# Kernel optimization log

Measured on AMD Instinct MI355X. Metric: run time of the kernel, lower is better.

## Reference

```python
import jax, jax.numpy as jnp
import numpy as np

N, C, L = 1024, 3, 6000
CONV_CH = [20, 32, 64, 20]
K = 3            # conv kernel size, padding (K-1)//2 = 1 -> SAME
POOL = 2
HID = 100
FLAT_DIM = (L // POOL**4 + 2 * C + 1) * CONV_CH[-1]  # (375 + 7) * 20 = 7640


def setup_inputs() -> dict:
    key = jax.random.key(0)
    ks = jax.random.split(key, 10)
    d = {"x": jax.random.normal(ks[0], (N, C, L), jnp.float32)}
    ins = [C] + CONV_CH[:-1]
    for i, (ic, oc) in enumerate(zip(ins, CONV_CH)):
        d[f"w{i}"] = jax.random.normal(ks[1 + i], (oc, ic, K), jnp.float32) * (1.0 / np.sqrt(ic * K))
        d[f"b{i}"] = jnp.zeros((oc,), jnp.float32)
    d["wc"] = jax.random.normal(ks[6], (CONV_CH[-1], C, 1), jnp.float32) * (1.0 / np.sqrt(C))
    d["bc"] = jnp.zeros((CONV_CH[-1],), jnp.float32)
    d["wl0"] = jax.random.normal(ks[7], (HID, FLAT_DIM), jnp.float32) * (1.0 / np.sqrt(FLAT_DIM))
    d["bl0"] = jnp.zeros((HID,), jnp.float32)
    d["wl1"] = jax.random.normal(ks[8], (2, HID), jnp.float32) * (1.0 / np.sqrt(HID))
    d["bl1"] = jnp.zeros((2,), jnp.float32)
    return d


def conv1d(x, w, b, pad):
    # x: (N, C_in, L), w: (C_out, C_in, K)
    out = jax.lax.conv_general_dilated(x, w, (1,), [(pad, pad)],
                                       dimension_numbers=('NCH', 'OIH', 'NCH'))
    return out + b[None, :, None]


def maxpool2(x):
    n, c, l = x.shape  # l always even here (6000 / 2^k)
    return x.reshape(n, c, l // 2, 2).max(-1)


def cov_eig_feats(x):
    # batched covariance as a single contraction (avoids the O(N*L*C*C) bmm intermediate)
    n, c, l = x.shape
    diff = x - x.mean(-1, keepdims=True)
    cov = jnp.einsum('ncl,ndl->ncd', diff, diff) / (l - 1)  # (N, C, C)
    # cov is symmetric PSD -> eigh (real); torch uses generic eig and keeps real parts
    vals, vecs = jnp.linalg.eigh(cov)
    vals = vals[..., None] / vals.max()          # global max over batch, like torch
    cov = cov / jnp.abs(cov).max()
    return jnp.concatenate([cov, vals, vecs], axis=-1)  # (N, C, 2C+1)


def reference(x, w0, b0, w1, b1, w2, b2, w3, b3, wc, bc, wl0, bl0, wl1, bl1):
    feats = jax.lax.stop_gradient(cov_eig_feats(x))  # torch branch is @no_grad
    h = x
    for w, b in ((w0, b0), (w1, b1), (w2, b2), (w3, b3)):
        h = maxpool2(jax.nn.relu(conv1d(h, w, b, (K - 1) // 2)))
    h = h.reshape(h.shape[0], -1)                    # (N, 20*375)
    h1 = jax.nn.relu(conv1d(feats, wc, bc, 0))       # (N, 20, 7)
    h1 = h1.reshape(h1.shape[0], -1)
    h = jnp.concatenate([h, h1], axis=1)             # (N, 7640)
    h = jax.nn.relu(h @ wl0.T + bl0)
    out = h @ wl1.T + bl1                            # (N, 2)
    return (out[:, :1], out[:, 1:])
```

## Files before the change

### kernel.cpp

```cpp
#include <hip/hip_runtime.h>
#include <hip/hip_bf16.h>
#include <hip/hip_fp16.h>
#include <math.h>

#define NBATCH 1024
#define LIN    6000
#define HCATW  7640
#define HID    100

#define TCH   54
#define NCHK  7

#define ASZ 3552
#define BSZ 8920

#define W0OFF 0
#define W1OFF 192
#define W2OFF 2112
#define W3OFF 8256
#define B0OFF 12352
#define B1OFF 12372
#define B2OFF 12404
#define B3OFF 12468
#define WREPSZ 12496

#define FCNS 4

__device__ __forceinline__ void pack_one(int idx, int OC, int IC, int OCG,
                                         int OPG, int WSTR,
                                         const float* __restrict__ w,
                                         float* __restrict__ dst)
{
    if (idx >= OCG * IC * WSTR) return;
    int ocg = idx / (IC * WSTR);
    int r   = idx - ocg * (IC * WSTR);
    int ic  = r / WSTR;
    int q   = r - ic * WSTR;
    int o   = q / 3, k = q - o * 3;
    int oc  = ocg * OPG + o;
    dst[idx] = (o < OPG && oc < OC) ? w[(oc * IC + ic) * 3 + k] : 0.f;
}

__global__ __launch_bounds__(256) void repack_kernel(
    const float* __restrict__ w0, const float* __restrict__ b0,
    const float* __restrict__ w1, const float* __restrict__ b1,
    const float* __restrict__ w2, const float* __restrict__ b2,
    const float* __restrict__ w3, const float* __restrict__ b3,
    float* __restrict__ wrep)
{
    int idx = blockIdx.x * 256 + threadIdx.x;
    pack_one(idx, 20,  3, 4, 5, 16, w0, wrep + W0OFF);
    pack_one(idx, 32, 20, 4, 8, 24, w1, wrep + W1OFF);
    pack_one(idx, 64, 32, 8, 8, 24, w2, wrep + W2OFF);
    pack_one(idx, 20, 64, 4, 5, 16, w3, wrep + W3OFF);
    if (idx < 20)            wrep[B0OFF + idx] = b0[idx];
    else if (idx < 52)  { int i = idx - 20;  wrep[B1OFF + i] = b1[i]; }
    else if (idx < 116) { int i = idx - 52;  wrep[B2OFF + i] = b2[i]; }
    else if (idx < 136) { int i = idx - 116; wrep[B3OFF + i] = b3[i]; }
}

template<int IC, int OC, int OCG, int OPG, int WSTR, int JOUT, int LG, int JBLK,
         bool IN16, bool OUT16, bool FINAL>
__device__ __forceinline__ void stage_eo(const float* __restrict__ in,
                                         float* __restrict__ out,
                                         float* __restrict__ outg,
                                         const float* __restrict__ wrep,
                                         const float* __restrict__ brep,
                                         int pbase, int o3, int wv, int lane,
                                         int zero)
{
    constexpr int PIN  = JOUT + 1;
    constexpr int POUT = JOUT / 2;
    constexpr int NJT  = (JOUT + 64 * JBLK - 1) / (64 * JBLK);
    for (int task = wv; task < OCG * NJT; task += 8) {
        const int ocg = task / NJT;
        const int jt  = task - ocg * NJT;
        const int j0  = jt * (64 * JBLK) + lane;
        const float* bp = brep + ocg * OPG;
        float ae[JBLK][OPG], ao[JBLK][OPG];
#pragma unroll
        for (int t = 0; t < JBLK; ++t)
#pragma unroll
            for (int o = 0; o < OPG; ++o) { ae[t][o] = bp[o]; ao[t][o] = ae[t][o]; }
        const float* wbase = wrep + ocg * (IC * WSTR) + zero;
#pragma unroll 2
        for (int ic = 0; ic < IC; ++ic) {
            const float* wp = wbase + ic * WSTR;
            float wr[WSTR];
#pragma unroll
            for (int q = 0; q < WSTR / 4; ++q)
                *(float4*)&wr[q * 4] = *(const float4*)(wp + q * 4);
#pragma unroll
            for (int t = 0; t < JBLK; ++t) {
                const int jj = j0 + t * 64;
                const int jc = (jj < JOUT) ? jj : (JOUT - 1);
                float e0, e1, o0, o1;
                if constexpr (IN16) {
                    const float* ipw = in + ic * PIN;
                    uint2 pw;
                    __builtin_memcpy(&pw, ipw + jc, 8);
                    __half2 h0 = *reinterpret_cast<const __half2*>(&pw.x);
                    __half2 h1 = *reinterpret_cast<const __half2*>(&pw.y);
                    e0 = __low2float(h0); o0 = __high2float(h0);
                    e1 = __low2float(h1); o1 = __high2float(h1);
                } else {
                    const float* ip = in + ic * (2 * PIN);
                    float2 ev, ov;
                    __builtin_memcpy(&ev, ip + jc, 8);
                    __builtin_memcpy(&ov, ip + PIN + jc, 8);
                    e0 = ev.x; e1 = ev.y;
                    o0 = ov.x; o1 = ov.y;
                }
#pragma unroll
                for (int o = 0; o < OPG; ++o) {
                    const float w0 = wr[o*3+0], w1 = wr[o*3+1], w2 = wr[o*3+2];
                    ae[t][o] = fmaf(e0, w0, fmaf(o0, w1, fmaf(e1, w2, ae[t][o])));
                    ao[t][o] = fmaf(o0, w0, fmaf(e1, w1, fmaf(o1, w2, ao[t][o])));
                }
            }
        }
#pragma unroll
        for (int t = 0; t < JBLK; ++t) {
            const int jj = j0 + t * 64;
            if constexpr (FINAL) {
                const int gj = o3 + jj;
                if (gj < 375 && jj < JOUT) {
#pragma unroll
                    for (int o = 0; o < OPG; ++o)
                        outg[(ocg*OPG+o) * 375 + gj] =
                            fmaxf(fmaxf(ae[t][o], ao[t][o]), 0.f);
                }
            } else {
                const int g = pbase + jj;
                const bool val = (jj < JOUT) && (g >= 0) && (g < LG);
                if (jj < JOUT) {
                    if constexpr (OUT16) {
                        __half* dh = (__half*)out;
#pragma unroll
                        for (int o = 0; o < OPG; ++o) {
                            float v = val ? fmaxf(fmaxf(ae[t][o], ao[t][o]), 0.f)
                                          : 0.f;
                            dh[(ocg*OPG+o) * JOUT + jj] = __float2half(v);
                        }
                    } else {
                        float* dst = out + ((jj & 1) ? POUT : 0) + (jj >> 1);
#pragma unroll
                        for (int o = 0; o < OPG; ++o)
                            dst[(ocg*OPG+o) * JOUT] =
                                val ? fmaxf(fmaxf(ae[t][o], ao[t][o]), 0.f) : 0.f;
                    }
                }
            }
        }
    }
}

__global__ __launch_bounds__(512, 6) void conv_chain_eo(
    const float* __restrict__ x,
    const float* __restrict__ wrep,
    float* __restrict__ hcat)
{
    __shared__ float A[ASZ];
    __shared__ float B[BSZ];

    const int tid  = threadIdx.x;
    const int wv   = __builtin_amdgcn_readfirstlane(tid >> 6);
    const int lane = tid & 63;
    const int zero = __builtin_amdgcn_ds_bpermute(0, 0);
    const int n     = blockIdx.x / NCHK;
    const int chunk = blockIdx.x % NCHK;
    const int o3 = chunk * TCH;
    const int p2 = 2*o3 - 1, p1 = 4*o3 - 3, p0 = 8*o3 - 7, xs = 16*o3 - 15;

    const float* xn = x + (size_t)n * 3 * LIN;
    for (int idx = tid; idx < 3 * 894; idx += 512) {
        int c = idx / 894, i = idx - c * 894;
        int g = xs + i;
        float v = (g >= 0 && g < LIN) ? xn[c * LIN + g] : 0.f;
        A[c * 894 + ((i & 1) ? 447 : 0) + (i >> 1)] = v;
    }
    __syncthreads();
    stage_eo< 3, 20, 4, 5, 16, 446, 3000, 2, false, false, false>(
        A, B, nullptr, wrep + W0OFF, wrep + B0OFF, p0, o3, wv, lane, zero);
    __syncthreads();
    stage_eo<20, 32, 4, 8, 24, 222, 1500, 2, false, true,  false>(
        B, A, nullptr, wrep + W1OFF, wrep + B1OFF, p1, o3, wv, lane, zero);
    __syncthreads();
    stage_eo<32, 64, 8, 8, 24, 110,  750, 2, true,  false, false>(
        A, B, nullptr, wrep + W2OFF, wrep + B2OFF, p2, o3, wv, lane, zero);
    __syncthreads();
    stage_eo<64, 20, 4, 5, 16,  54,  375, 1, false, false, true >(
        B, nullptr, hcat + (size_t)n * HCATW,
        wrep + W3OFF, wrep + B3OFF, o3, o3, wv, lane, zero);
}

__device__ __forceinline__ float fsign(float a, float b) {
    return (b >= 0.0f) ? fabsf(a) : -fabsf(a);
}
__device__ __forceinline__ float slapy2(float xx, float yy) {
    float xa = fabsf(xx), ya = fabsf(yy);
    float w = fmaxf(xa, ya), z = fminf(xa, ya);
    if (z == 0.f) return w;
    float t = z / w;
    return w * sqrtf(1.f + t*t);
}
__device__ __forceinline__ void slartg(float f, float g, float& c, float& s, float& r) {
    if (g == 0.f)      { c = 1.f; s = 0.f; r = f; }
    else if (f == 0.f) { c = 0.f; s = (g >= 0.f ? 1.f : -1.f); r = fabsf(g); }
    else {
        float d = sqrtf(f*f + g*g);
        c = fabsf(f) / d;
        r = fsign(d, f);
        s = g / r;
    }
}
__device__ void slaev2(float a, float b, float cc,
                       float& rt1, float& rt2, float& cs1, float& sn1) {
    float sm = a + cc, df = a - cc;
    float adf = fabsf(df);
    float tb = b + b, ab = fabsf(tb);
    float acmx, acmn;
    if (fabsf(a) > fabsf(cc)) { acmx = a; acmn = cc; } else { acmx = cc; acmn = a; }
    float rt;
    if (adf > ab)      { float t = ab/adf; rt = adf*sqrtf(1.f + t*t); }
    else if (adf < ab) { float t = adf/ab; rt = ab*sqrtf(1.f + t*t); }
    else rt = ab * sqrtf(2.f);
    int sgn1;
    if (sm < 0.f)      { rt1 = 0.5f*(sm - rt); sgn1 = -1; rt2 = (acmx/rt1)*acmn - (b/rt1)*b; }
    else if (sm > 0.f) { rt1 = 0.5f*(sm + rt); sgn1 =  1; rt2 = (acmx/rt1)*acmn - (b/rt1)*b; }
    else               { rt1 = 0.5f*rt; rt2 = -0.5f*rt; sgn1 = 1; }
    float cs; int sgn2;
    if (df >= 0.f) { cs = df + rt; sgn2 = 1; } else { cs = df - rt; sgn2 = -1; }
    float acs = fabsf(cs);
    if (acs > ab) {
        float ct = -tb / cs;
        sn1 = 1.f / sqrtf(1.f + ct*ct);
        cs1 = ct * sn1;
    } else {
        if (ab == 0.f) { cs1 = 1.f; sn1 = 0.f; }
        else {
            float tn = -cs / tb;
            cs1 = 1.f / sqrtf(1.f + tn*tn);
            sn1 = tn * cs1;
        }
    }
    if (sgn1 == sgn2) { float tn = cs1; cs1 = -sn1; sn1 = tn; }
}
__device__ __forceinline__ void rot_cols(float z[3][3], int jc, float c, float s) {
    for (int i = 0; i < 3; ++i) {
        float t = z[i][jc+1];
        z[i][jc+1] = c*t - s*z[i][jc];
        z[i][jc]   = s*t + c*z[i][jc];
    }
}

__device__ void ssteqr3(float d[3], float e[2], float z[3][3]) {
    const float eps    = 5.9604645e-8f;
    const float eps2   = eps * eps;
    const float safmin = 1.17549435e-38f;
    const int n = 3;
    for (int i = 0; i < 3; ++i)
        for (int j = 0; j < 3; ++j) z[i][j] = (i == j) ? 1.f : 0.f;
    const int nmaxit = n * 30;
    int jtot = 0;
    float cw[2], sw[2];
    int l1 = 1, l, m, lend, lsv, lendsv;

L10:
    if (l1 > n) goto L160;
    if (l1 > 1) e[l1-2] = 0.f;
    if (l1 <= n-1) {
        for (m = l1; m <= n-1; ++m) {
            float tst = fabsf(e[m-1]);
            if (tst == 0.f) goto L30;
            if (tst <= (sqrtf(fabsf(d[m-1])) * sqrtf(fabsf(d[m]))) * eps) {
                e[m-1] = 0.f;
                goto L30;
            }
        }
    }
    m = n;
L30:
    l = l1; lsv = l; lend = m; lendsv = lend; l1 = m + 1;
    if (lend == l) goto L10;
    if (fabsf(d[lend-1]) < fabsf(d[l-1])) { lend = lsv; l = lendsv; }
    if (lend > l) {
L40:
        if (l != lend) {
            bool found = false;
            for (m = l; m <= lend-1; ++m) {
                float tst = e[m-1]*e[m-1];
                if (tst <= (eps2*fabsf(d[m-1]))*fabsf(d[m]) + safmin) { found = true; break; }
            }
            if (!found) m = lend;
        } else m = lend;
        if (m < lend) e[m-1] = 0.f;
        {
            float p = d[l-1];
            if (m == l) {
                d[l-1] = p;
                l = l + 1;
                if (l <= lend) goto L40;
                goto L140;
            }
            if (m == l+1) {
                float rt1, rt2, c2, s2;
                slaev2(d[l-1], e[l-1], d[l], rt1, rt2, c2, s2);
                rot_cols(z, l-1, c2, s2);
                d[l-1] = rt1; d[l] = rt2; e[l-1] = 0.f;
                l += 2;
                if (l <= lend) goto L40;
                goto L140;
            }
            if (jtot == nmaxit) goto L140;
            jtot++;
            float g = (d[l] - p) / (2.f * e[l-1]);
            float r = slapy2(g, 1.f);
            g = d[m-1] - p + e[l-1] / (g + fsign(r, g));
            float s = 1.f, c = 1.f;
            p = 0.f;
            for (int i = m-1; i >= l; --i) {
                float f = s * e[i-1];
                float b = c * e[i-1];
                slartg(g, f, c, s, r);
                if (i != m-1) e[i] = r;
                g = d[i] - p;
                r = (d[i-1] - g)*s + 2.f*c*b;
                p = s * r;
                d[i] = g + p;
                g = c*r - b;
                cw[i-l] = c; sw[i-l] = -s;
            }
            for (int jj = m-l; jj >= 1; --jj)
                rot_cols(z, l + jj - 2, cw[jj-1], sw[jj-1]);
            d[l-1] = d[l-1] - p;
            e[l-1] = g;
            goto L40;
        }
    } else {
L90:
        if (l != lend) {
            bool found = false;
            for (m = l; m >= lend+1; --m) {
                float tst = e[m-2]*e[m-2];
                if (tst <= (eps2*fabsf(d[m-1]))*fabsf(d[m-2]) + safmin) { found = true; break; }
            }
            if (!found) m = lend;
        } else m = lend;
        if (m > lend) e[m-2] = 0.f;
        {
            float p = d[l-1];
            if (m == l) {
                d[l-1] = p;
                l = l - 1;
                if (l >= lend) goto L90;
                goto L140;
            }
            if (m == l-1) {
                float rt1, rt2, c2, s2;
                slaev2(d[l-2], e[l-2], d[l-1], rt1, rt2, c2, s2);
                rot_cols(z, l-2, c2, s2);
                d[l-2] = rt1; d[l-1] = rt2; e[l-2] = 0.f;
                l -= 2;
                if (l >= lend) goto L90;
                goto L140;
            }
            if (jtot == nmaxit) goto L140;
            jtot++;
            float g = (d[l-2] - p) / (2.f * e[l-2]);
            float r = slapy2(g, 1.f);
            g = d[m-1] - p + e[l-2] / (g + fsign(r, g));
            float s = 1.f, c = 1.f;
            p = 0.f;
            for (int i = m; i <= l-1; ++i) {
                float f = s * e[i-1];
                float b = c * e[i-1];
                slartg(g, f, c, s, r);
                if (i != m) e[i-2] = r;
                g = d[i-1] - p;
                r = (d[i] - g)*s + 2.f*c*b;
                p = s * r;
                d[i-1] = g + p;
                g = c*r - b;
                cw[i-m] = c; sw[i-m] = s;
            }
            for (int jj = 1; jj <= l-m; ++jj)
                rot_cols(z, m + jj - 2, cw[jj-1], sw[jj-1]);
            d[l-1] = d[l-1] - p;
            e[l-2] = g;
            goto L90;
        }
    }
L140:
    if (jtot < nmaxit) goto L10;
L160:
    for (int ii = 2; ii <= n; ++ii) {
        int i = ii - 1, k = i;
        float p = d[i-1];
        for (int j = ii; j <= n; ++j)
            if (d[j-1] < p) { k = j; p = d[j-1]; }
        if (k != i) {
            d[k-1] = d[i-1]; d[i-1] = p;
            for (int r0 = 0; r0 < 3; ++r0) {
                float t = z[r0][i-1]; z[r0][i-1] = z[r0][k-1]; z[r0][k-1] = t;
            }
        }
    }
}

__global__ __launch_bounds__(256) void cov_eig_kernel(const float* __restrict__ x,
                                                      float* __restrict__ eigbuf,
                                                      unsigned int* __restrict__ gmax)
{
    __shared__ float part[4][9];
    const int n = blockIdx.x;
    const float* xn = x + (size_t)n * 3 * LIN;
    float v[9] = {0,0,0,0,0,0,0,0,0};
    for (int l = threadIdx.x; l < LIN; l += 256) {
        float a = xn[l], b = xn[LIN + l], c = xn[2*LIN + l];
        v[0] += a; v[1] += b; v[2] += c;
        v[3] = fmaf(a,a,v[3]); v[4] = fmaf(a,b,v[4]); v[5] = fmaf(a,c,v[5]);
        v[6] = fmaf(b,b,v[6]); v[7] = fmaf(b,c,v[7]); v[8] = fmaf(c,c,v[8]);
    }
#pragma unroll
    for (int off = 32; off > 0; off >>= 1)
#pragma unroll
        for (int i = 0; i < 9; ++i) v[i] += __shfl_down(v[i], off, 64);
    const int wv = threadIdx.x >> 6, lane = threadIdx.x & 63;
    if (lane == 0)
        for (int i = 0; i < 9; ++i) part[wv][i] = v[i];
    __syncthreads();
    if (threadIdx.x == 0) {
        float t[9];
        for (int i = 0; i < 9; ++i)
            t[i] = part[0][i] + part[1][i] + part[2][i] + part[3][i];
        const float Lf = (float)LIN;
        float m0 = t[0]/Lf, m1 = t[1]/Lf, m2 = t[2]/Lf;
        float c00 = (t[3] - Lf*m0*m0) / (Lf - 1.f);
        float c01 = (t[4] - Lf*m0*m1) / (Lf - 1.f);
        float c02 = (t[5] - Lf*m0*m2) / (Lf - 1.f);
        float c11 = (t[6] - Lf*m1*m1) / (Lf - 1.f);
        float c12 = (t[7] - Lf*m1*m2) / (Lf - 1.f);
        float c22 = (t[8] - Lf*m2*m2) / (Lf - 1.f);

        float dd[3], ee[2], tau, v2;
        {
            float a21 = c01, a31 = c02, a22 = c11, a32 = c12, a33 = c22;
            float xnorm = fabsf(a31);
            if (xnorm == 0.f) {
                tau = 0.f; v2 = 0.f;
                dd[0] = c00; dd[1] = a22; dd[2] = a33;
                ee[0] = a21; ee[1] = a32;
            } else {
                float beta = -fsign(slapy2(a21, xnorm), a21);
                tau = (beta - a21) / beta;
                v2  = a31 / (a21 - beta);
                ee[0] = beta;
                float x1 = tau*(a22 + a32*v2);
                float x2 = tau*(a32 + a33*v2);
                float al = -0.5f*tau*(x1 + x2*v2);
                float w1 = x1 + al;
                float w2 = x2 + al*v2;
                a22 -= 2.f*w1;
                a32 -= (v2*w1 + w2);
                a33 -= 2.f*v2*w2;
                dd[0] = c00; dd[1] = a22; dd[2] = a33;
                ee[1] = a32;
            }
        }
        float zz[3][3];
        ssteqr3(dd, ee, zz);
        if (tau != 0.f) {
            for (int j = 0; j < 3; ++j) {
                float sum = zz[1][j] + v2*zz[2][j];
                zz[1][j] -= tau * sum;
                zz[2][j] -= tau * v2 * sum;
            }
        }

        float* eb = eigbuf + n * 21;
        eb[0] = c00; eb[1] = c01; eb[2] = c02;
        eb[3] = c01; eb[4] = c11; eb[5] = c12;
        eb[6] = c02; eb[7] = c12; eb[8] = c22;
        eb[9] = dd[0]; eb[10] = dd[1]; eb[11] = dd[2];
        for (int c = 0; c < 3; ++c)
            for (int k = 0; k < 3; ++k) eb[12 + c*3 + k] = zz[c][k];

        float vmax = fmaxf(dd[0], fmaxf(dd[1], dd[2]));
        float cmax = 0.f;
        for (int i = 0; i < 9; ++i) cmax = fmaxf(cmax, fabsf(eb[i]));
        atomicMax(&gmax[0], __float_as_uint(vmax));
        atomicMax(&gmax[1], __float_as_uint(cmax));
    }
}

__global__ __launch_bounds__(256) void feats_kernel(const float* __restrict__ eigbuf,
                                                    const unsigned int* __restrict__ gmax,
                                                    const float* __restrict__ wc,
                                                    const float* __restrict__ bc,
                                                    float* __restrict__ hcat)
{
    const int n = blockIdx.x;
    const int t = threadIdx.x;
    if (t >= 140) return;
    const int o = t / 7, j = t % 7;
    const float* eb = eigbuf + n * 21;
    const float vmax = __uint_as_float(gmax[0]);
    const float cmax = __uint_as_float(gmax[1]);
    float f0, f1, f2;
    if (j < 3)       { f0 = eb[0*3+j]/cmax; f1 = eb[1*3+j]/cmax; f2 = eb[2*3+j]/cmax; }
    else if (j == 3) { f0 = eb[9]/vmax;     f1 = eb[10]/vmax;    f2 = eb[11]/vmax; }
    else             { int k = j-4; f0 = eb[12+0*3+k]; f1 = eb[12+1*3+k]; f2 = eb[12+2*3+k]; }
    float r = bc[o] + wc[o*3+0]*f0 + wc[o*3+1]*f1 + wc[o*3+2]*f2;
    hcat[(size_t)n*HCATW + 7500 + o*7 + j] = fmaxf(r, 0.f);
}

__global__ __launch_bounds__(512) void fc01_kernel(const float* __restrict__ hcat,
                                                   const float* __restrict__ wl0,
                                                   const float* __restrict__ bl0,
                                                   const float* __restrict__ wl1,
                                                   const float* __restrict__ bl1,
                                                   float* __restrict__ out)
{
    __shared__ float hl[FCNS * HCATW];
    __shared__ float hbuf[FCNS * HID];
    const int tid = threadIdx.x;
    const int n0 = blockIdx.x * FCNS;
    for (int i = tid; i < FCNS * (HCATW/4); i += 512) {
        int s  = i / (HCATW/4);
        int k4 = i - s * (HCATW/4);
        ((float4*)hl)[s * (HCATW/4) + k4] =
            *(const float4*)(hcat + (size_t)(n0 + s) * HCATW + k4 * 4);
    }
    __syncthreads();
    const int wv = tid >> 6;
    const int lane = tid & 63;
    for (int ot = wv; ot < HID / 4; ot += 8) {
        float acc[4][FCNS];
#pragma unroll
        for (int oo = 0; oo < 4; ++oo)
#pragma unroll
            for (int s = 0; s < FCNS; ++s) acc[oo][s] = 0.f;
        for (int k = lane * 4; k < HCATW; k += 256) {
            float4 hv[FCNS];
#pragma unroll
            for (int s = 0; s < FCNS; ++s)
                hv[s] = *(const float4*)(hl + s * HCATW + k);
#pragma unroll
            for (int oo = 0; oo < 4; ++oo) {
                const float4 w4 = *(const float4*)(wl0 + (size_t)(ot*4+oo) * HCATW + k);
#pragma unroll
                for (int s = 0; s < FCNS; ++s) {
                    acc[oo][s] = fmaf(hv[s].x, w4.x, acc[oo][s]);
                    acc[oo][s] = fmaf(hv[s].y, w4.y, acc[oo][s]);
                    acc[oo][s] = fmaf(hv[s].z, w4.z, acc[oo][s]);
                    acc[oo][s] = fmaf(hv[s].w, w4.w, acc[oo][s]);
                }
            }
        }
#pragma unroll
        for (int off = 32; off > 0; off >>= 1)
#pragma unroll
            for (int oo = 0; oo < 4; ++oo)
#pragma unroll
                for (int s = 0; s < FCNS; ++s)
                    acc[oo][s] += __shfl_down(acc[oo][s], off, 64);
        if (lane == 0) {
#pragma unroll
            for (int oo = 0; oo < 4; ++oo) {
                const float b = bl0[ot*4+oo];
#pragma unroll
                for (int s = 0; s < FCNS; ++s)
                    hbuf[s * HID + ot*4+oo] = fmaxf(acc[oo][s] + b, 0.f);
            }
        }
    }
    __syncthreads();
    if (tid < 2 * FCNS) {
        const int s = tid >> 1, r = tid & 1;
        const float* w = wl1 + r * HID;
        float acc = bl1[r];
        for (int k = 0; k < HID; ++k) acc = fmaf(hbuf[s * HID + k], w[k], acc);
        out[r * NBATCH + n0 + s] = acc;
    }
}

extern "C" void kernel_launch(void* const* d_in, const int* in_sizes, int n_in,
                              void* d_out, int out_size, void* d_ws, size_t ws_size,
                              hipStream_t stream)
{
    const float* x   = (const float*)d_in[0];
    const float* w0  = (const float*)d_in[1];
    const float* b0  = (const float*)d_in[2];
    const float* w1  = (const float*)d_in[3];
    const float* b1  = (const float*)d_in[4];
    const float* w2  = (const float*)d_in[5];
    const float* b2  = (const float*)d_in[6];
    const float* w3  = (const float*)d_in[7];
    const float* b3  = (const float*)d_in[8];
    const float* wc  = (const float*)d_in[9];
    const float* bc  = (const float*)d_in[10];
    const float* wl0 = (const float*)d_in[11];
    const float* bl0 = (const float*)d_in[12];
    const float* wl1 = (const float*)d_in[13];
    const float* bl1 = (const float*)d_in[14];
    float* out = (float*)d_out;

    const size_t HCAT_N = (size_t)NBATCH * HCATW;
    const size_t EIG_N  = (size_t)NBATCH * 21;
    const size_t need_bytes = (HCAT_N + EIG_N + 4 + WREPSZ) * 4 + 16;
    if (ws_size < need_bytes) return;

    float* ws     = (float*)d_ws;
    float* hcat   = ws;
    float* eigbuf = hcat + HCAT_N;
    unsigned int* gmax = (unsigned int*)(eigbuf + EIG_N);
    float* wrep   = (float*)(gmax + 4);

    hipMemsetAsync(gmax, 0, 2 * sizeof(unsigned int), stream);

    repack_kernel<<<24, 256, 0, stream>>>(w0, b0, w1, b1, w2, b2, w3, b3, wrep);
    conv_chain_eo<<<NBATCH * NCHK, 512, 0, stream>>>(x, wrep, hcat);
    cov_eig_kernel<<<NBATCH, 256, 0, stream>>>(x, eigbuf, gmax);
    feats_kernel<<<NBATCH, 256, 0, stream>>>(eigbuf, gmax, wc, bc, hcat);
    fc01_kernel<<<NBATCH / FCNS, 512, 0, stream>>>(hcat, wl0, bl0, wl1, bl1, out);
}
```

Before: 704.1 us.

## Use packed fp16 dot2 for middle conv stages and split final stage across waves

Stages 1 and 2 now use packed fp16 weights with v_dot2_f32_f16, computing two taps per instruction from half-precision activations. Stage 0 now writes fp16 output, which shrinks the shared buffer. The final conv stage splits the input channels across two wave halves and reduces the partial sums through shared memory, so all 8 waves do work instead of 4. This cuts ALU instruction count and LDS footprint, at the cost of extra fp16 rounding of weights and activations.

After: 652.0 us. -7.4%, faster.

```diff
diff --git a/kernel.cpp b/kernel.cpp
--- a/kernel.cpp
+++ b/kernel.cpp
@@ -12,19 +12,34 @@
 #define NCHK  7
 
 #define ASZ 3552
-#define BSZ 8920
+#define BSZ 7040
 
 #define W0OFF 0
 #define W1OFF 192
-#define W2OFF 2112
-#define W3OFF 8256
-#define B0OFF 12352
-#define B1OFF 12372
-#define B2OFF 12404
-#define B3OFF 12468
-#define WREPSZ 12496
+#define W2OFF 1472
+#define W3OFF 5568
+#define B0OFF 9664
+#define B1OFF 9684
+#define B2OFF 9716
+#define B3OFF 9780
+#define WREPSZ 9800
 
 #define FCNS 4
+
+typedef _Float16 v2h __attribute__((ext_vector_type(2)));
+
+__device__ __forceinline__ float fdot2_f16(unsigned int a, unsigned int b, float c) {
+#if __has_builtin(__builtin_amdgcn_fdot2)
+    v2h ah, bh;
+    __builtin_memcpy(&ah, &a, 4);
+    __builtin_memcpy(&bh, &b, 4);
+    return __builtin_amdgcn_fdot2(ah, bh, c, false);
+#else
+    float d;
+    asm("v_dot2_f32_f16 %0, %1, %2, %3" : "=v"(d) : "v"(a), "v"(b), "v"(c));
+    return d;
+#endif
+}
 
 __device__ __forceinline__ void pack_one(int idx, int OC, int IC, int OCG,
                                          int OPG, int WSTR,
@@ -41,6 +56,27 @@
     dst[idx] = (o < OPG && oc < OC) ? w[(oc * IC + ic) * 3 + k] : 0.f;
 }
 
+__device__ __forceinline__ void pack_pk(int idx, int OC, int IC,
+                                        const float* __restrict__ w,
+                                        unsigned int* __restrict__ dst)
+{
+    const int OCG = OC >> 3;
+    if (idx >= OCG * IC * 16) return;
+    int ocg = idx / (IC * 16);
+    int r   = idx - ocg * (IC * 16);
+    int ic  = r >> 4, q = r & 15;
+    int o   = q & 7;
+    int oc  = ocg * 8 + o;
+    const float* ws = w + (oc * IC + ic) * 3;
+    if (q < 8) {
+        unsigned int lo = __half_as_ushort(__float2half(ws[0]));
+        unsigned int hi = __half_as_ushort(__float2half(ws[1]));
+        dst[idx] = lo | (hi << 16);
+    } else {
+        dst[idx] = __float_as_uint(ws[2]);
+    }
+}
+
 __global__ __launch_bounds__(256) void repack_kernel(
     const float* __restrict__ w0, const float* __restrict__ b0,
     const float* __restrict__ w1, const float* __restrict__ b1,
@@ -49,9 +85,10 @@
     float* __restrict__ wrep)
 {
     int idx = blockIdx.x * 256 + threadIdx.x;
+    unsigned int* wu = (unsigned int*)wrep;
     pack_one(idx, 20,  3, 4, 5, 16, w0, wrep + W0OFF);
-    pack_one(idx, 32, 20, 4, 8, 24, w1, wrep + W1OFF);
-    pack_one(idx, 64, 32, 8, 8, 24, w2, wrep + W2OFF);
+    pack_pk (idx, 32, 20, w1, wu + W1OFF);
+    pack_pk (idx, 64, 32, w2, wu + W2OFF);
     pack_one(idx, 20, 64, 4, 5, 16, w3, wrep + W3OFF);
     if (idx < 20)            wrep[B0OFF + idx] = b0[idx];
     else if (idx < 52)  { int i = idx - 20;  wrep[B1OFF + i] = b1[i]; }
@@ -60,7 +97,7 @@
 }
 
 template<int IC, int OC, int OCG, int OPG, int WSTR, int JOUT, int LG, int JBLK,
-         bool IN16, bool OUT16, bool FINAL>
+         bool IN16, bool OUT16, bool PKW, bool FINAL>
 __device__ __forceinline__ void stage_eo(const float* __restrict__ in,
                                          float* __restrict__ out,
                                          float* __restrict__ outg,
@@ -94,28 +131,46 @@
             for (int t = 0; t < JBLK; ++t) {
                 const int jj = j0 + t * 64;
                 const int jc = (jj < JOUT) ? jj : (JOUT - 1);
-                float e0, e1, o0, o1;
-                if constexpr (IN16) {
+                if constexpr (PKW) {
                     const float* ipw = in + ic * PIN;
                     uint2 pw;
                     __builtin_memcpy(&pw, ipw + jc, 8);
-                    __half2 h0 = *reinterpret_cast<const __half2*>(&pw.x);
-                    __half2 h1 = *reinterpret_cast<const __half2*>(&pw.y);
-                    e0 = __low2float(h0); o0 = __high2float(h0);
-                    e1 = __low2float(h1); o1 = __high2float(h1);
+                    const unsigned int crossu = (pw.x >> 16) | (pw.y << 16);
+                    v2h h1; __builtin_memcpy(&h1, &pw.y, 4);
+                    const float e1 = (float)h1.x, o1 = (float)h1.y;
+#pragma unroll
+                    for (int o = 0; o < OPG; ++o) {
+                        const unsigned int wpk = __float_as_uint(wr[o]);
+                        const float w2 = wr[8 + o];
+                        ae[t][o] = fdot2_f16(pw.x,  wpk, ae[t][o]);
+                        ao[t][o] = fdot2_f16(crossu, wpk, ao[t][o]);
+                        ae[t][o] = fmaf(e1, w2, ae[t][o]);
+                        ao[t][o] = fmaf(o1, w2, ao[t][o]);
+                    }
                 } else {
-                    const float* ip = in + ic * (2 * PIN);
-                    float2 ev, ov;
-                    __builtin_memcpy(&ev, ip + jc, 8);
-                    __builtin_memcpy(&ov, ip + PIN + jc, 8);
-                    e0 = ev.x; e1 = ev.y;
-                    o0 = ov.x; o1 = ov.y;
-                }
-#pragma unroll
-                for (int o = 0; o < OPG; ++o) {
-                    const float w0 = wr[o*3+0], w1 = wr[o*3+1], w2 = wr[o*3+2];
-                    ae[t][o] = fmaf(e0, w0, fmaf(o0, w1, fmaf(e1, w2, ae[t][o])));
-                    ao[t][o] = fmaf(o0, w0, fmaf(e1, w1, fmaf(o1, w2, ao[t][o])));
+                    float e0, e1, o0, o1;
+                    if constexpr (IN16) {
+                        const float* ipw = in + ic * PIN;
+                        uint2 pw;
+                        __builtin_memcpy(&pw, ipw + jc, 8);
+                        __half2 h0 = *reinterpret_cast<const __half2*>(&pw.x);
+                        __half2 h1 = *reinterpret_cast<const __half2*>(&pw.y);
+                        e0 = __low2float(h0); o0 = __high2float(h0);
+                        e1 = __low2float(h1); o1 = __high2float(h1);
+                    } else {
+                        const float* ip = in + ic * (2 * PIN);
+                        float2 ev, ov;
+                        __builtin_memcpy(&ev, ip + jc, 8);
+                        __builtin_memcpy(&ov, ip + PIN + jc, 8);
+                        e0 = ev.x; e1 = ev.y;
+                        o0 = ov.x; o1 = ov.y;
+                    }
+#pragma unroll
+                    for (int o = 0; o < OPG; ++o) {
+                        const float w0 = wr[o*3+0], w1 = wr[o*3+1], w2 = wr[o*3+2];
+                        ae[t][o] = fmaf(e0, w0, fmaf(o0, w1, fmaf(e1, w2, ae[t][o])));
+                        ao[t][o] = fmaf(o0, w0, fmaf(e1, w1, fmaf(o1, w2, ao[t][o])));
+                    }
                 }
             }
         }
@@ -155,6 +210,68 @@
     }
 }
 
+__device__ __forceinline__ void stage3_split(const float* __restrict__ in,
+                                             float* __restrict__ part,
+                                             float* __restrict__ outg,
+                                             const float* __restrict__ wrep,
+                                             const float* __restrict__ brep,
+                                             int o3, int wv, int lane, int zero)
+{
+    constexpr int JOUT = 54, PIN = 55, OPG = 5, WSTR = 16;
+    const int ocg = wv & 3, ih = wv >> 2;
+    const int j  = lane;
+    const int jc = (j < JOUT) ? j : (JOUT - 1);
+    const float* bp = brep + ocg * OPG;
+    float ae[OPG], ao[OPG];
+#pragma unroll
+    for (int o = 0; o < OPG; ++o) {
+        float b = ih ? 0.f : bp[o];
+        ae[o] = b; ao[o] = b;
+    }
+    const float* wbase = wrep + (ocg * 64 + ih * 32) * WSTR + zero;
+#pragma unroll 2
+    for (int ic = 0; ic < 32; ++ic) {
+        const float* ip = in + (ih * 32 + ic) * (2 * PIN);
+        float2 ev, ov;
+        __builtin_memcpy(&ev, ip + jc, 8);
+        __builtin_memcpy(&ov, ip + PIN + jc, 8);
+        const float* wp = wbase + ic * WSTR;
+        float wr[WSTR];
+#pragma unroll
+        for (int q = 0; q < WSTR / 4; ++q)
+            *(float4*)&wr[q * 4] = *(const float4*)(wp + q * 4);
+#pragma unroll
+        for (int o = 0; o < OPG; ++o) {
+            const float w0 = wr[o*3+0], w1 = wr[o*3+1], w2 = wr[o*3+2];
+            ae[o] = fmaf(ev.x, w0, fmaf(ov.x, w1, fmaf(ev.y, w2, ae[o])));
+            ao[o] = fmaf(ov.x, w0, fmaf(ev.y, w1, fmaf(ov.y, w2, ao[o])));
+        }
+    }
+    if (ih == 1) {
+#pragma unroll
+        for (int o = 0; o < OPG; ++o) {
+            float2 p = make_float2(ae[o], ao[o]);
+            __builtin_memcpy(part + (ocg * OPG + o) * 128 + lane * 2, &p, 8);
+        }
+    }
+    __syncthreads();
+    if (ih == 0) {
+#pragma unroll
+        for (int o = 0; o < OPG; ++o) {
+            float2 p;
+            __builtin_memcpy(&p, part + (ocg * OPG + o) * 128 + lane * 2, 8);
+            ae[o] += p.x; ao[o] += p.y;
+        }
+        const int gj = o3 + j;
+        if (gj < 375 && j < JOUT) {
+#pragma unroll
+            for (int o = 0; o < OPG; ++o)
+                outg[(ocg * OPG + o) * 375 + gj] =
+                    fmaxf(fmaxf(ae[o], ao[o]), 0.f);
+        }
+    }
+}
+
 __global__ __launch_bounds__(512, 6) void conv_chain_eo(
     const float* __restrict__ x,
     const float* __restrict__ wrep,
@@ -180,18 +297,17 @@
         A[c * 894 + ((i & 1) ? 447 : 0) + (i >> 1)] = v;
     }
     __syncthreads();
-    stage_eo< 3, 20, 4, 5, 16, 446, 3000, 2, false, false, false>(
+    stage_eo< 3, 20, 4, 5, 16, 446, 3000, 2, false, true,  false, false>(
         A, B, nullptr, wrep + W0OFF, wrep + B0OFF, p0, o3, wv, lane, zero);
     __syncthreads();
-    stage_eo<20, 32, 4, 8, 24, 222, 1500, 2, false, true,  false>(
+    stage_eo<20, 32, 4, 8, 16, 222, 1500, 2, true,  true,  true,  false>(
         B, A, nullptr, wrep + W1OFF, wrep + B1OFF, p1, o3, wv, lane, zero);
     __syncthreads();
-    stage_eo<32, 64, 8, 8, 24, 110,  750, 2, true,  false, false>(
+    stage_eo<32, 64, 8, 8, 16, 110,  750, 2, true,  false, true,  false>(
         A, B, nullptr, wrep + W2OFF, wrep + B2OFF, p2, o3, wv, lane, zero);
     __syncthreads();
-    stage_eo<64, 20, 4, 5, 16,  54,  375, 1, false, false, true >(
-        B, nullptr, hcat + (size_t)n * HCATW,
-        wrep + W3OFF, wrep + B3OFF, o3, o3, wv, lane, zero);
+    stage3_split(B, A, hcat + (size_t)n * HCATW,
+                 wrep + W3OFF, wrep + B3OFF, o3, wv, lane, zero);
 }
 
 __device__ __forceinline__ float fsign(float a, float b) {
@@ -619,7 +735,7 @@
 
     hipMemsetAsync(gmax, 0, 2 * sizeof(unsigned int), stream);
 
-    repack_kernel<<<24, 256, 0, stream>>>(w0, b0, w1, b1, w2, b2, w3, b3, wrep);
+    repack_kernel<<<16, 256, 0, stream>>>(w0, b0, w1, b1, w2, b2, w3, b3, wrep);
     conv_chain_eo<<<NBATCH * NCHK, 512, 0, stream>>>(x, wrep, hcat);
     cov_eig_kernel<<<NBATCH, 256, 0, stream>>>(x, eigbuf, gmax);
     feats_kernel<<<NBATCH, 256, 0, stream>>>(eigbuf, gmax, wc, bc, hcat);
```
